# Performance work log

Hardware: AMD Instinct MI355X
Metric: run time of the kernel (lower is better)

## Reference

```python
import jax, jax.numpy as jnp
import numpy as np

EPS = 1e-5
NUM_HEADS = 8


def _conv_transpose_3x3_s2(x, w):
    # x: [B,Cin,H,W], w: [Cin,Cout,3,3] (torch ConvTranspose2d layout), stride 2, no padding
    # output spatial = (H-1)*2 + 3 = 2H+1
    return jax.lax.conv_transpose(
        x, w, strides=(2, 2), padding='VALID',
        dimension_numbers=('NCHW', 'IOHW', 'NCHW'))


def setup_inputs() -> dict:
    key = jax.random.key(0)
    ks = jax.random.split(key, 8)
    B, C, H, W = 4, 256, 32, 32
    Co, Dk, Dv = 128, 64, 64
    s = 0.05
    return {
        'x': jax.random.normal(ks[0], (B, C, H, W), jnp.float32),
        'gamma': jnp.ones((C,), jnp.float32),
        'beta': jnp.zeros((C,), jnp.float32),
        'running_mean': jax.random.normal(ks[1], (C,), jnp.float32) * 0.1,
        'running_var': jax.random.uniform(ks[2], (C,), jnp.float32, 0.5, 1.5),
        'w_sc': jax.random.normal(ks[3], (C, Co, 3, 3), jnp.float32) * s,
        'w_q': jax.random.normal(ks[4], (C, Dk, 3, 3), jnp.float32) * s,
        'w_k': jax.random.normal(ks[5], (Dk, C), jnp.float32) * s,
        'w_v': jax.random.normal(ks[6], (Dv, C), jnp.float32) * s,
        'w_o': jax.random.normal(ks[7], (Co, Dv), jnp.float32) * s,
    }


def reference(x, gamma, beta, running_mean, running_var, w_sc, w_q, w_k, w_v, w_o):
    B, C, H, W = x.shape
    h = NUM_HEADS
    # BatchNorm (inference, running stats) + ReLU, shared by both branches
    inv = jax.lax.rsqrt(running_var + EPS)
    xn = (x - running_mean[None, :, None, None]) * (gamma * inv)[None, :, None, None] \
         + beta[None, :, None, None]
    xr = jax.nn.relu(xn)

    # Shortcut: ConvTranspose2d(C->Co, 3, stride 2) -> [B,Co,2H+1,2W+1]
    shortcut = _conv_transpose_3x3_s2(xr, w_sc)

    # Attention branch ('UP'): query upsampled via ConvTranspose, k/v 1x1 at low res
    q = _conv_transpose_3x3_s2(xr, w_q)              # [B,Dk,Hu,Wu]
    k = jnp.einsum('dc,bchw->bdhw', w_k, xr)         # [B,Dk,H,W]
    v = jnp.einsum('dc,bchw->bdhw', w_v, xr)         # [B,Dv,H,W]
    Hu, Wu = q.shape[2], q.shape[3]
    Nq, Nk = Hu * Wu, H * W
    Dk, Dv = q.shape[1], v.shape[1]
    dk = Dk // h
    qh = q.reshape(B, h, dk, Nq)
    kh = k.reshape(B, h, dk, Nk)
    vh = v.reshape(B, h, Dv // h, Nk)
    scores = jnp.einsum('bhdq,bhdk->bhqk', qh, kh) / jnp.sqrt(jnp.float32(dk))
    attn = jax.nn.softmax(scores, axis=-1)           # use_softmax=True
    out = jnp.einsum('bhqk,bhdk->bhdq', attn, vh)    # [B,h,dv,Nq]
    out = out.reshape(B, Dv, Hu, Wu)
    out = jnp.einsum('od,bdhw->bohw', w_o, out)      # 1x1 output projection -> Co

    return shortcut + out
```

## Files before the change

### kernel.cpp

```cpp
#include <hip/hip_runtime.h>

typedef unsigned short u16;
typedef unsigned int u32;

typedef float f4 __attribute__((ext_vector_type(4)));
typedef short s8v __attribute__((ext_vector_type(8)));
typedef u16 us8 __attribute__((ext_vector_type(8)));
typedef _Float16 h4 __attribute__((ext_vector_type(4)));
typedef __fp16 g2 __attribute__((ext_vector_type(2)));

__device__ __forceinline__ u16 f2bf(float x){ u32 b=__float_as_uint(x); b += 0x7FFFu + ((b>>16)&1u); return (u16)(b>>16); }
__device__ __forceinline__ u16 f2h(float x){ union{_Float16 h; u16 u;} c; c.h=(_Float16)x; return c.u; }

#define O_XRT  2101248u
#define O_WPT  (O_XRT + 2097152u)
#define O_QH   (O_WPT + 884736u)
#define O_KT   (O_QH  + 2163200u)
#define O_V    (O_KT  + 524288u)
#define O_ATT  (O_V   + 524288u)
#define O_WKV  (O_ATT + 2163200u)
#define O_WO2  (O_WKV + 65536u)

__global__ __launch_bounds__(256) void k_prep(
    const float* __restrict__ x, const float* __restrict__ gamma, const float* __restrict__ beta,
    const float* __restrict__ mean, const float* __restrict__ var,
    const float* __restrict__ w_sc, const float* __restrict__ w_q,
    const float* __restrict__ w_k, const float* __restrict__ w_v, const float* __restrict__ w_o,
    u16* __restrict__ xrT, u16* __restrict__ wpt,
    u16* __restrict__ wkv, u16* __restrict__ wo2)
{
  __shared__ float SS[128], SH[128];
  __shared__ __align__(16) u16 T[32*136];
  int bi = blockIdx.x, tid = threadIdx.x;
  if (bi < 256) {
    int b = bi >> 6, pt = (bi >> 1) & 31, ch = bi & 1;
    int pix0 = pt*32, c0 = ch*128;
    if (tid < 128) {
      int c = c0 + tid;
      float s = gamma[c]*rsqrtf(var[c] + 1e-5f);
      SS[tid] = s; SH[tid] = beta[c] - mean[c]*s;
    }
    __syncthreads();
    int pix_l = tid & 31, c_l = tid >> 5;
    #pragma unroll 4
    for (int it = 0; it < 16; ++it) {
      int cl = it*8 + c_l;
      float v = x[(((size_t)(b*256 + c0 + cl))<<10) + pix0 + pix_l];
      T[pix_l*136 + cl] = f2bf(fmaxf(v*SS[cl] + SH[cl], 0.f));
    }
    __syncthreads();
    int pix_r = tid >> 3, j = tid & 7;
    us8 v0 = *(const us8*)(T + pix_r*136 + j*8);
    us8 v1 = *(const us8*)(T + pix_r*136 + 64 + j*8);
    u16* dst = xrT + (((size_t)(b*1024 + pix0 + pix_r))<<8) + c0;
    *(us8*)(dst + j*8) = v0;
    *(us8*)(dst + 64 + j*8) = v1;
    return;
  }
  int wid = (bi - 256)*256 + tid;
  if (wid < 442368) {
    int c, m, ky, kx; float val;
    if (wid < 294912) {
      c = wid / 1152; int r = wid - c*1152; m = r / 9; int t9 = r - m*9; ky = t9/3; kx = t9 - ky*3;
      val = w_sc[wid];
    } else {
      int i2 = wid - 294912;
      c = i2 / 576; int r = i2 - c*576; m = r / 9; int t9 = r - m*9; ky = t9/3; kx = t9 - ky*3;
      val = w_q[i2] * 0.51007023f;
      m += 128;
    }
    int py = (ky==1) ? 1 : 0; int dy = (ky==0) ? 1 : 0;
    int px = (kx==1) ? 1 : 0; int dx = (kx==0) ? 1 : 0;
    int cls = py*2 + px;
    int tt, KP, base;
    if (cls==0){ tt = dy*2+dx; KP=1024; base=0; }
    else if (cls==1){ tt = dy; KP=512; base=196608; }
    else if (cls==2){ tt = dx; KP=512; base=294912; }
    else { tt = 0; KP=256; base=393216; }
    wpt[base + m*KP + tt*256 + c] = f2bf(val);
  } else if (wid < 475136) {
    int i = wid - 442368; int m = i >> 8, c = i & 255;
    float vv = (m < 64) ? w_k[m*256 + c] : w_v[(m-64)*256 + c];
    wkv[m*256 + c] = f2bf(vv);
  } else if (wid < 483328) {
    int i = wid - 475136;
    wo2[i] = f2bf(w_o[i]);
  }
}

template<int PY,int PX,int TT>
__device__ __forceinline__ void conv_cls(
    const u16* __restrict__ xrT, const u16* __restrict__ wcls,
    float* __restrict__ outF, u16* __restrict__ qh,
    int mb, int nb, u16* Blds)
{
  constexpr int Hy = 33 - PY, Wx = 33 - PX;
  constexpr int NC = 4*Hy*Wx;
  constexpr int KP = TT*256;
  constexpr int NKT = KP/32;
  int tid = threadIdx.x;
  int lane = tid & 63, wv = tid >> 6, quad = lane >> 4, c15 = lane & 15;
  int sn = tid >> 2, sg = tid & 3;
  int n_g = nb*64 + sn;
  bool nv = n_g < NC;
  int bb=0, yq=0, xq=0;
  if (nv) { bb = n_g/(Hy*Wx); int rem = n_g - bb*(Hy*Wx); yq = rem/Wx; xq = rem - yq*Wx; }
  f4 acc[4];
  #pragma unroll
  for (int i=0;i<4;i++) acc[i] = (f4){0.f,0.f,0.f,0.f};
  const u16* arow = wcls + (size_t)(mb*64 + wv*16 + c15)*KP + quad*8;
  auto loadB = [&](int kt)->us8 {
    int tt = kt >> 3, cb = (kt & 7)*32;
    int dy, dx;
    if (TT==4){ dy = tt>>1; dx = tt&1; }
    else if (TT==2){ if (PX==1){ dy=tt; dx=0; } else { dy=0; dx=tt; } }
    else { dy=0; dx=0; }
    int ii = yq - dy, jj = xq - dx;
    bool ok = nv && (ii>=0) && (ii<32) && (jj>=0) && (jj<32);
    us8 v = (us8)0;
    if (ok) v = *(const us8*)(xrT + (((size_t)((bb<<10) + ii*32 + jj))<<8) + cb + sg*8);
    return v;
  };
  us8 cur = loadB(0);
  for (int kt = 0; kt < NKT; ++kt) {
    __syncthreads();
    *(us8*)(Blds + sn*40 + sg*8) = cur;
    __syncthreads();
    if (kt + 1 < NKT) cur = loadB(kt + 1);
    s8v a = *(const s8v*)(arow + kt*32);
    #pragma unroll
    for (int t4=0;t4<4;t4++) {
      s8v bf = *(const s8v*)(Blds + (t4*16 + c15)*40 + quad*8);
      acc[t4] = __builtin_amdgcn_mfma_f32_16x16x32_bf16(a, bf, acc[t4], 0, 0, 0);
    }
  }
  #pragma unroll
  for (int t4=0;t4<4;t4++) {
    int n2 = nb*64 + t4*16 + c15;
    if (n2 < NC) {
      int bb2 = n2/(Hy*Wx); int rem = n2 - bb2*(Hy*Wx); int yq2 = rem/Wx; int xq2 = rem - yq2*Wx;
      int pix = (2*yq2 + PY)*65 + (2*xq2 + PX);
      if (mb < 2) {
        int mrow = mb*64 + wv*16 + quad*4;
        #pragma unroll
        for (int rg=0; rg<4; rg++)
          outF[(size_t)(bb2*128 + mrow + rg)*4225 + pix] = acc[t4][rg];
      } else {
        int dv = wv*16 + quad*4;
        u16 pk[4];
        #pragma unroll
        for (int rg=0; rg<4; rg++) pk[rg] = f2h(acc[t4][rg]);
        *(uint2*)(qh + (((size_t)(bb2*4225 + pix))<<6) + dv) = *(uint2*)pk;
      }
    }
  }
}

__global__ __launch_bounds__(256) void k_conv(
    const u16* __restrict__ xrT, const u16* __restrict__ wpt, const u16* __restrict__ wkv,
    float* __restrict__ outF, u16* __restrict__ qh,
    u16* __restrict__ kT, u16* __restrict__ vbuf)
{
  __shared__ __align__(16) u16 Blds[64*40];
  int bi = blockIdx.x;
  if (bi < 795) {
    int mb = bi % 3, cy = bi / 3;
    if (cy < 69)       conv_cls<0,0,4>(xrT, wpt,          outF, qh, mb, cy,     Blds);
    else if (cy < 135) conv_cls<0,1,2>(xrT, wpt + 196608, outF, qh, mb, cy-69,  Blds);
    else if (cy < 201) conv_cls<1,0,2>(xrT, wpt + 294912, outF, qh, mb, cy-135, Blds);
    else               conv_cls<1,1,1>(xrT, wpt + 393216, outF, qh, mb, cy-201, Blds);
    return;
  }
  int t = bi - 795;
  int mb = t & 1, nb = t >> 1;
  int tid = threadIdx.x;
  int lane = tid & 63, wv = tid >> 6, quad = lane >> 4, c15 = lane & 15;
  int sn = tid >> 2, sg = tid & 3;
  int n_g = nb*64 + sn;
  f4 acc[4];
  #pragma unroll
  for (int i=0;i<4;i++) acc[i] = (f4){0.f,0.f,0.f,0.f};
  const u16* arow = wkv + (size_t)(mb*64 + wv*16 + c15)*256 + quad*8;
  us8 cur = *(const us8*)(xrT + (((size_t)n_g)<<8) + sg*8);
  for (int kt = 0; kt < 8; ++kt) {
    __syncthreads();
    *(us8*)(Blds + sn*40 + sg*8) = cur;
    __syncthreads();
    if (kt < 7) cur = *(const us8*)(xrT + (((size_t)n_g)<<8) + (kt+1)*32 + sg*8);
    s8v a = *(const s8v*)(arow + kt*32);
    #pragma unroll
    for (int t4=0;t4<4;t4++) {
      s8v bf = *(const s8v*)(Blds + (t4*16 + c15)*40 + quad*8);
      acc[t4] = __builtin_amdgcn_mfma_f32_16x16x32_bf16(a, bf, acc[t4], 0, 0, 0);
    }
  }
  int ml = wv*16 + quad*4;
  #pragma unroll
  for (int t4=0;t4<4;t4++) {
    int n2 = nb*64 + t4*16 + c15;
    int b = n2 >> 10, pix = n2 & 1023;
    if (mb == 0) {
      int h = ml >> 3, d0 = ml & 7;
      u16 pk[4];
      #pragma unroll
      for (int rg=0; rg<4; rg++) pk[rg] = f2h(acc[t4][rg]);
      *(uint2*)(kT + ((size_t)(b*8+h)<<13) + pix*8 + d0) = *(uint2*)pk;
    } else {
      #pragma unroll
      for (int rg=0; rg<4; rg++)
        vbuf[(((size_t)(b*64 + ml + rg))<<10) + pix] = f2h(acc[t4][rg]);
    }
  }
}

__global__ __launch_bounds__(256) void k_attn(
    const u16* __restrict__ qh, const u16* __restrict__ kT, const u16* __restrict__ vbuf,
    u16* __restrict__ attT)
{
  __shared__ __align__(16) u16 KL[8192];
  __shared__ __align__(16) u16 VL[9*1032];
  int qt = blockIdx.x, bh = blockIdx.y;
  int b = bh >> 3, h = bh & 7;
  int tid = threadIdx.x, lane = tid & 63, wv = tid >> 6, quad = lane >> 4, c15 = lane & 15;
  {
    const uint4* kg = (const uint4*)(kT + ((size_t)bh << 13));
    for (int i = tid; i < 1024; i += 256) ((uint4*)KL)[i] = kg[i];
    const u16* vg = vbuf + ((size_t)(b*64 + h*8) << 10);
    for (int i = tid; i < 1024; i += 256) {
      int dv = i >> 7, k8 = (i & 127) << 3;
      *(uint4*)(VL + dv*1032 + k8) = *(const uint4*)(vg + (dv<<10) + k8);
    }
    if (tid < 129) {
      us8 ones;
      #pragma unroll
      for (int i=0;i<8;i++) ones[i] = 0x3C00;
      *(us8*)(VL + 8*1032 + tid*8) = ones;
    }
  }
  __syncthreads();
  int q0 = qt*128 + wv*32 + c15;
  int q1 = q0 + 16;
  int qa = q0 < 4224 ? q0 : 4224;
  int qb = q1 < 4224 ? q1 : 4224;
  uint2 t0 = *(const uint2*)(qh + (((size_t)(b*4225 + qa))<<6) + h*8 + (quad&1)*4);
  uint2 t1 = *(const uint2*)(qh + (((size_t)(b*4225 + qb))<<6) + h*8 + (quad&1)*4);
  h4 bq0 = quad < 2 ? *(h4*)&t0 : (h4)(_Float16)0.f;
  h4 bq1 = quad < 2 ? *(h4*)&t1 : (h4)(_Float16)0.f;
  const u16* klb = KL + c15*8 + (quad&1)*4;
  int vr = c15 > 8 ? 8 : c15;
  const u16* vlb = VL + vr*1032 + quad*4;
  const f4 zf = {0.f,0.f,0.f,0.f};
  f4 O0 = {0.f,0.f,0.f,0.f}, O1 = {0.f,0.f,0.f,0.f};
  #pragma unroll 8
  for (int kt=0; kt<64; ++kt) {
    h4 ak = *(const h4*)(klb + kt*128);
    h4 av = *(const h4*)(vlb + kt*16);
    f4 s0 = __builtin_amdgcn_mfma_f32_16x16x16f16(ak, bq0, zf, 0, 0, 0);
    f4 s1 = __builtin_amdgcn_mfma_f32_16x16x16f16(ak, bq1, zf, 0, 0, 0);
    g2 p0l = __builtin_amdgcn_cvt_pkrtz(__builtin_amdgcn_exp2f(s0[0]), __builtin_amdgcn_exp2f(s0[1]));
    g2 p0h = __builtin_amdgcn_cvt_pkrtz(__builtin_amdgcn_exp2f(s0[2]), __builtin_amdgcn_exp2f(s0[3]));
    g2 p1l = __builtin_amdgcn_cvt_pkrtz(__builtin_amdgcn_exp2f(s1[0]), __builtin_amdgcn_exp2f(s1[1]));
    g2 p1h = __builtin_amdgcn_cvt_pkrtz(__builtin_amdgcn_exp2f(s1[2]), __builtin_amdgcn_exp2f(s1[3]));
    h4 pf0; pf0[0]=(_Float16)p0l[0]; pf0[1]=(_Float16)p0l[1]; pf0[2]=(_Float16)p0h[0]; pf0[3]=(_Float16)p0h[1];
    h4 pf1; pf1[0]=(_Float16)p1l[0]; pf1[1]=(_Float16)p1l[1]; pf1[2]=(_Float16)p1h[0]; pf1[3]=(_Float16)p1h[1];
    O0 = __builtin_amdgcn_mfma_f32_16x16x16f16(av, pf0, O0, 0, 0, 0);
    O1 = __builtin_amdgcn_mfma_f32_16x16x16f16(av, pf1, O1, 0, 0, 0);
  }
  float l0 = __shfl(O0[0], 32 + c15, 64);
  float l1 = __shfl(O1[0], 32 + c15, 64);
  float r0 = __builtin_amdgcn_rcpf(l0);
  float r1 = __builtin_amdgcn_rcpf(l1);
  if (quad < 2) {
    if (q0 < 4225) {
      u16 pk[4];
      #pragma unroll
      for (int rg=0;rg<4;rg++) pk[rg] = f2bf(O0[rg]*r0);
      *(uint2*)(attT + (((size_t)(b*4225 + q0))<<6) + h*8 + quad*4) = *(uint2*)pk;
    }
    if (q1 < 4225) {
      u16 pk[4];
      #pragma unroll
      for (int rg=0;rg<4;rg++) pk[rg] = f2bf(O1[rg]*r1);
      *(uint2*)(attT + (((size_t)(b*4225 + q1))<<6) + h*8 + quad*4) = *(uint2*)pk;
    }
  }
}

__global__ __launch_bounds__(256) void k_proj(
    const u16* __restrict__ attT, const u16* __restrict__ wo2, float* __restrict__ outF)
{
  int nbi = blockIdx.x, b = blockIdx.y;
  int tid = threadIdx.x;
  int lane = tid & 63, wv = tid >> 6, quad = lane >> 4, c15 = lane & 15;
  f4 acc[2][4];
  #pragma unroll
  for (int am=0;am<2;am++)
    #pragma unroll
    for (int i=0;i<4;i++) acc[am][i] = (f4){0.f,0.f,0.f,0.f};
  #pragma unroll
  for (int kt = 0; kt < 2; ++kt) {
    s8v a0 = *(const s8v*)(wo2 + (size_t)(wv*32 + c15)*64 + kt*32 + quad*8);
    s8v a1 = *(const s8v*)(wo2 + (size_t)(wv*32 + 16 + c15)*64 + kt*32 + quad*8);
    #pragma unroll
    for (int t4=0;t4<4;t4++) {
      int n = nbi*64 + t4*16 + c15;
      int nc = n < 4224 ? n : 4224;
      s8v bf = *(const s8v*)(attT + (((size_t)(b*4225 + nc))<<6) + kt*32 + quad*8);
      acc[0][t4] = __builtin_amdgcn_mfma_f32_16x16x32_bf16(a0, bf, acc[0][t4], 0, 0, 0);
      acc[1][t4] = __builtin_amdgcn_mfma_f32_16x16x32_bf16(a1, bf, acc[1][t4], 0, 0, 0);
    }
  }
  #pragma unroll
  for (int am=0;am<2;am++) {
    int mrow = wv*32 + am*16 + quad*4;
    #pragma unroll
    for (int t4=0;t4<4;t4++) {
      int n2 = nbi*64 + t4*16 + c15;
      if (n2 < 4225) {
        float* op = outF + (size_t)(b*128 + mrow)*4225 + n2;
        #pragma unroll
        for (int rg=0; rg<4; rg++) op[(size_t)rg*4225] += acc[am][t4][rg];
      }
    }
  }
}

extern "C" void kernel_launch(void* const* d_in, const int* in_sizes, int n_in,
                              void* d_out, int out_size, void* d_ws, size_t ws_size,
                              hipStream_t stream) {
  const float* x     = (const float*)d_in[0];
  const float* gamma = (const float*)d_in[1];
  const float* beta  = (const float*)d_in[2];
  const float* mean  = (const float*)d_in[3];
  const float* var   = (const float*)d_in[4];
  const float* w_sc  = (const float*)d_in[5];
  const float* w_q   = (const float*)d_in[6];
  const float* w_k   = (const float*)d_in[7];
  const float* w_v   = (const float*)d_in[8];
  const float* w_o   = (const float*)d_in[9];
  char* ws = (char*)d_ws;
  u16*   xrT  = (u16*)(ws + O_XRT);
  u16*   wpt  = (u16*)(ws + O_WPT);
  u16*   qhb  = (u16*)(ws + O_QH);
  u16*   kT   = (u16*)(ws + O_KT);
  u16*   vbuf = (u16*)(ws + O_V);
  u16*   attT = (u16*)(ws + O_ATT);
  u16*   wkv  = (u16*)(ws + O_WKV);
  u16*   wo2  = (u16*)(ws + O_WO2);
  float* outF = (float*)d_out;

  k_prep<<<2144, 256, 0, stream>>>(x, gamma, beta, mean, var, w_sc, w_q, w_k, w_v, w_o,
                                   xrT, wpt, wkv, wo2);
  k_conv<<<923, 256, 0, stream>>>(xrT, wpt, wkv, outF, qhb, kT, vbuf);
  k_attn<<<dim3(34, 32), 256, 0, stream>>>(qhb, kT, vbuf, attT);
  k_proj<<<dim3(67, 4), 256, 0, stream>>>(attT, wo2, outF);
}
```

Baseline: 136.0 us.

## Pad activation buffer with zero halo and double-buffer K=64 LDS tiles in conv

The transposed activations are stored in a zero-padded 34x34 layout, with the border zeroed by extra prep blocks. This lets the conv gather drop its per-load bounds checks and predication. The conv and k/v GEMM loops now consume 64 channels per step with double-buffered LDS, so each iteration needs one barrier instead of two and there are half as many iterations. The attention loop also builds its P fragment by bit-casting instead of converting element by element. The cost is more LDS per block, which may limit occupancy, plus the extra prep work to zero the halo.

```diff
diff --git a/kernel.cpp b/kernel.cpp
--- a/kernel.cpp
+++ b/kernel.cpp
@@ -12,8 +12,8 @@
 __device__ __forceinline__ u16 f2bf(float x){ u32 b=__float_as_uint(x); b += 0x7FFFu + ((b>>16)&1u); return (u16)(b>>16); }
 __device__ __forceinline__ u16 f2h(float x){ union{_Float16 h; u16 u;} c; c.h=(_Float16)x; return c.u; }
 
-#define O_XRT  2101248u
-#define O_WPT  (O_XRT + 2097152u)
+#define O_XRT  4096u
+#define O_WPT  (O_XRT + 2367488u)
 #define O_QH   (O_WPT + 884736u)
 #define O_KT   (O_QH  + 2163200u)
 #define O_V    (O_KT  + 524288u)
@@ -26,7 +26,7 @@
     const float* __restrict__ mean, const float* __restrict__ var,
     const float* __restrict__ w_sc, const float* __restrict__ w_q,
     const float* __restrict__ w_k, const float* __restrict__ w_v, const float* __restrict__ w_o,
-    u16* __restrict__ xrT, u16* __restrict__ wpt,
+    u16* __restrict__ xrTp, u16* __restrict__ wpt,
     u16* __restrict__ wkv, u16* __restrict__ wo2)
 {
   __shared__ float SS[128], SH[128];
@@ -52,7 +52,7 @@
     int pix_r = tid >> 3, j = tid & 7;
     us8 v0 = *(const us8*)(T + pix_r*136 + j*8);
     us8 v1 = *(const us8*)(T + pix_r*136 + 64 + j*8);
-    u16* dst = xrT + (((size_t)(b*1024 + pix0 + pix_r))<<8) + c0;
+    u16* dst = xrTp + (((size_t)(b*1156 + (pt+1)*34 + 1 + pix_r))<<8) + c0;
     *(us8*)(dst + j*8) = v0;
     *(us8*)(dst + 64 + j*8) = v1;
     return;
@@ -85,60 +85,75 @@
   } else if (wid < 483328) {
     int i = wid - 475136;
     wo2[i] = f2bf(w_o[i]);
+  } else if (wid < 500224) {
+    int i = wid - 483328;
+    int b = i / 4224; int r = i - b*4224;
+    int hp = r >> 5, j = r & 31;
+    int p;
+    if (hp < 34) p = hp;
+    else if (hp < 68) p = 33*34 + (hp - 34);
+    else if (hp < 100) p = (hp - 68 + 1)*34;
+    else p = (hp - 100 + 1)*34 + 33;
+    *(us8*)(xrTp + (((size_t)(b*1156 + p))<<8) + j*8) = (us8)0;
   }
 }
 
 template<int PY,int PX,int TT>
 __device__ __forceinline__ void conv_cls(
-    const u16* __restrict__ xrT, const u16* __restrict__ wcls,
+    const u16* __restrict__ xrTp, const u16* __restrict__ wcls,
     float* __restrict__ outF, u16* __restrict__ qh,
     int mb, int nb, u16* Blds)
 {
   constexpr int Hy = 33 - PY, Wx = 33 - PX;
   constexpr int NC = 4*Hy*Wx;
   constexpr int KP = TT*256;
-  constexpr int NKT = KP/32;
+  constexpr int NKT = KP/64;
   int tid = threadIdx.x;
   int lane = tid & 63, wv = tid >> 6, quad = lane >> 4, c15 = lane & 15;
   int sn = tid >> 2, sg = tid & 3;
   int n_g = nb*64 + sn;
-  bool nv = n_g < NC;
-  int bb=0, yq=0, xq=0;
-  if (nv) { bb = n_g/(Hy*Wx); int rem = n_g - bb*(Hy*Wx); yq = rem/Wx; xq = rem - yq*Wx; }
+  int ncl = n_g < NC ? n_g : NC-1;
+  int bb = ncl/(Hy*Wx); int rem = ncl - bb*(Hy*Wx); int yq = rem/Wx; int xq = rem - yq*Wx;
+  const u16* bsrc = xrTp + (((size_t)(bb*1156 + (yq+1)*34 + xq+1))<<8) + sg*16;
   f4 acc[4];
   #pragma unroll
   for (int i=0;i<4;i++) acc[i] = (f4){0.f,0.f,0.f,0.f};
   const u16* arow = wcls + (size_t)(mb*64 + wv*16 + c15)*KP + quad*8;
-  auto loadB = [&](int kt)->us8 {
-    int tt = kt >> 3, cb = (kt & 7)*32;
+  auto loadB = [&](int kt, us8& v0, us8& v1) {
+    int tt = kt >> 2, c0 = (kt & 3)*64;
     int dy, dx;
     if (TT==4){ dy = tt>>1; dx = tt&1; }
     else if (TT==2){ if (PX==1){ dy=tt; dx=0; } else { dy=0; dx=tt; } }
     else { dy=0; dx=0; }
-    int ii = yq - dy, jj = xq - dx;
-    bool ok = nv && (ii>=0) && (ii<32) && (jj>=0) && (jj<32);
-    us8 v = (us8)0;
-    if (ok) v = *(const us8*)(xrT + (((size_t)((bb<<10) + ii*32 + jj))<<8) + cb + sg*8);
-    return v;
+    const u16* p = bsrc - (((dy*34+dx))<<8) + c0;
+    v0 = *(const us8*)p;
+    v1 = *(const us8*)(p+8);
   };
-  us8 cur = loadB(0);
+  us8 cv0, cv1; loadB(0, cv0, cv1);
+  int pb = 0;
   for (int kt = 0; kt < NKT; ++kt) {
+    u16* Bw = Blds + pb*4608;
+    *(us8*)(Bw + sn*72 + sg*16) = cv0;
+    *(us8*)(Bw + sn*72 + sg*16 + 8) = cv1;
     __syncthreads();
-    *(us8*)(Blds + sn*40 + sg*8) = cur;
-    __syncthreads();
-    if (kt + 1 < NKT) cur = loadB(kt + 1);
-    s8v a = *(const s8v*)(arow + kt*32);
+    if (kt + 1 < NKT) loadB(kt+1, cv0, cv1);
+    s8v a0 = *(const s8v*)(arow + kt*64);
+    s8v a1 = *(const s8v*)(arow + kt*64 + 32);
     #pragma unroll
     for (int t4=0;t4<4;t4++) {
-      s8v bf = *(const s8v*)(Blds + (t4*16 + c15)*40 + quad*8);
-      acc[t4] = __builtin_amdgcn_mfma_f32_16x16x32_bf16(a, bf, acc[t4], 0, 0, 0);
-    }
+      const u16* br = Blds + pb*4608 + (t4*16 + c15)*72 + quad*8;
+      s8v bf0 = *(const s8v*)br;
+      s8v bf1 = *(const s8v*)(br + 32);
+      acc[t4] = __builtin_amdgcn_mfma_f32_16x16x32_bf16(a0, bf0, acc[t4], 0, 0, 0);
+      acc[t4] = __builtin_amdgcn_mfma_f32_16x16x32_bf16(a1, bf1, acc[t4], 0, 0, 0);
+    }
+    pb ^= 1;
   }
   #pragma unroll
   for (int t4=0;t4<4;t4++) {
     int n2 = nb*64 + t4*16 + c15;
     if (n2 < NC) {
-      int bb2 = n2/(Hy*Wx); int rem = n2 - bb2*(Hy*Wx); int yq2 = rem/Wx; int xq2 = rem - yq2*Wx;
+      int bb2 = n2/(Hy*Wx); int rem2 = n2 - bb2*(Hy*Wx); int yq2 = rem2/Wx; int xq2 = rem2 - yq2*Wx;
       int pix = (2*yq2 + PY)*65 + (2*xq2 + PX);
       if (mb < 2) {
         int mrow = mb*64 + wv*16 + quad*4;
@@ -157,18 +172,18 @@
 }
 
 __global__ __launch_bounds__(256) void k_conv(
-    const u16* __restrict__ xrT, const u16* __restrict__ wpt, const u16* __restrict__ wkv,
+    const u16* __restrict__ xrTp, const u16* __restrict__ wpt, const u16* __restrict__ wkv,
     float* __restrict__ outF, u16* __restrict__ qh,
     u16* __restrict__ kT, u16* __restrict__ vbuf)
 {
-  __shared__ __align__(16) u16 Blds[64*40];
+  __shared__ __align__(16) u16 Blds[2*4608];
   int bi = blockIdx.x;
   if (bi < 795) {
     int mb = bi % 3, cy = bi / 3;
-    if (cy < 69)       conv_cls<0,0,4>(xrT, wpt,          outF, qh, mb, cy,     Blds);
-    else if (cy < 135) conv_cls<0,1,2>(xrT, wpt + 196608, outF, qh, mb, cy-69,  Blds);
-    else if (cy < 201) conv_cls<1,0,2>(xrT, wpt + 294912, outF, qh, mb, cy-135, Blds);
-    else               conv_cls<1,1,1>(xrT, wpt + 393216, outF, qh, mb, cy-201, Blds);
+    if (cy < 69)       conv_cls<0,0,4>(xrTp, wpt,          outF, qh, mb, cy,     Blds);
+    else if (cy < 135) conv_cls<0,1,2>(xrTp, wpt + 196608, outF, qh, mb, cy-69,  Blds);
+    else if (cy < 201) conv_cls<1,0,2>(xrTp, wpt + 294912, outF, qh, mb, cy-135, Blds);
+    else               conv_cls<1,1,1>(xrTp, wpt + 393216, outF, qh, mb, cy-201, Blds);
     return;
   }
   int t = bi - 795;
@@ -177,22 +192,31 @@
   int lane = tid & 63, wv = tid >> 6, quad = lane >> 4, c15 = lane & 15;
   int sn = tid >> 2, sg = tid & 3;
   int n_g = nb*64 + sn;
+  int b0 = n_g >> 10, pix0 = n_g & 1023, y0 = pix0 >> 5, x0 = pix0 & 31;
+  const u16* bsrc = xrTp + (((size_t)(b0*1156 + (y0+1)*34 + x0+1))<<8) + sg*16;
   f4 acc[4];
   #pragma unroll
   for (int i=0;i<4;i++) acc[i] = (f4){0.f,0.f,0.f,0.f};
   const u16* arow = wkv + (size_t)(mb*64 + wv*16 + c15)*256 + quad*8;
-  us8 cur = *(const us8*)(xrT + (((size_t)n_g)<<8) + sg*8);
-  for (int kt = 0; kt < 8; ++kt) {
+  us8 cv0 = *(const us8*)bsrc, cv1 = *(const us8*)(bsrc + 8);
+  int pb = 0;
+  for (int kt = 0; kt < 4; ++kt) {
+    u16* Bw = Blds + pb*4608;
+    *(us8*)(Bw + sn*72 + sg*16) = cv0;
+    *(us8*)(Bw + sn*72 + sg*16 + 8) = cv1;
     __syncthreads();
-    *(us8*)(Blds + sn*40 + sg*8) = cur;
-    __syncthreads();
-    if (kt < 7) cur = *(const us8*)(xrT + (((size_t)n_g)<<8) + (kt+1)*32 + sg*8);
-    s8v a = *(const s8v*)(arow + kt*32);
+    if (kt < 3) { cv0 = *(const us8*)(bsrc + (kt+1)*64); cv1 = *(const us8*)(bsrc + (kt+1)*64 + 8); }
+    s8v a0 = *(const s8v*)(arow + kt*64);
+    s8v a1 = *(const s8v*)(arow + kt*64 + 32);
     #pragma unroll
     for (int t4=0;t4<4;t4++) {
-      s8v bf = *(const s8v*)(Blds + (t4*16 + c15)*40 + quad*8);
-      acc[t4] = __builtin_amdgcn_mfma_f32_16x16x32_bf16(a, bf, acc[t4], 0, 0, 0);
-    }
+      const u16* br = Blds + pb*4608 + (t4*16 + c15)*72 + quad*8;
+      s8v bf0 = *(const s8v*)br;
+      s8v bf1 = *(const s8v*)(br + 32);
+      acc[t4] = __builtin_amdgcn_mfma_f32_16x16x32_bf16(a0, bf0, acc[t4], 0, 0, 0);
+      acc[t4] = __builtin_amdgcn_mfma_f32_16x16x32_bf16(a1, bf1, acc[t4], 0, 0, 0);
+    }
+    pb ^= 1;
   }
   int ml = wv*16 + quad*4;
   #pragma unroll
@@ -251,6 +275,7 @@
   const u16* vlb = VL + vr*1032 + quad*4;
   const f4 zf = {0.f,0.f,0.f,0.f};
   f4 O0 = {0.f,0.f,0.f,0.f}, O1 = {0.f,0.f,0.f,0.f};
+  union HU { uint2 u; h4 h; };
   #pragma unroll 8
   for (int kt=0; kt<64; ++kt) {
     h4 ak = *(const h4*)(klb + kt*128);
@@ -261,10 +286,10 @@
     g2 p0h = __builtin_amdgcn_cvt_pkrtz(__builtin_amdgcn_exp2f(s0[2]), __builtin_amdgcn_exp2f(s0[3]));
     g2 p1l = __builtin_amdgcn_cvt_pkrtz(__builtin_amdgcn_exp2f(s1[0]), __builtin_amdgcn_exp2f(s1[1]));
     g2 p1h = __builtin_amdgcn_cvt_pkrtz(__builtin_amdgcn_exp2f(s1[2]), __builtin_amdgcn_exp2f(s1[3]));
-    h4 pf0; pf0[0]=(_Float16)p0l[0]; pf0[1]=(_Float16)p0l[1]; pf0[2]=(_Float16)p0h[0]; pf0[3]=(_Float16)p0h[1];
-    h4 pf1; pf1[0]=(_Float16)p1l[0]; pf1[1]=(_Float16)p1l[1]; pf1[2]=(_Float16)p1h[0]; pf1[3]=(_Float16)p1h[1];
-    O0 = __builtin_amdgcn_mfma_f32_16x16x16f16(av, pf0, O0, 0, 0, 0);
-    O1 = __builtin_amdgcn_mfma_f32_16x16x16f16(av, pf1, O1, 0, 0, 0);
+    HU u0; u0.u.x = __builtin_bit_cast(u32, p0l); u0.u.y = __builtin_bit_cast(u32, p0h);
+    HU u1; u1.u.x = __builtin_bit_cast(u32, p1l); u1.u.y = __builtin_bit_cast(u32, p1h);
+    O0 = __builtin_amdgcn_mfma_f32_16x16x16f16(av, u0.h, O0, 0, 0, 0);
+    O1 = __builtin_amdgcn_mfma_f32_16x16x16f16(av, u1.h, O1, 0, 0, 0);
   }
   float l0 = __shfl(O0[0], 32 + c15, 64);
   float l1 = __shfl(O1[0], 32 + c15, 64);
@@ -339,7 +364,7 @@
   const float* w_v   = (const float*)d_in[8];
   const float* w_o   = (const float*)d_in[9];
   char* ws = (char*)d_ws;
-  u16*   xrT  = (u16*)(ws + O_XRT);
+  u16*   xrTp = (u16*)(ws + O_XRT);
   u16*   wpt  = (u16*)(ws + O_WPT);
   u16*   qhb  = (u16*)(ws + O_QH);
   u16*   kT   = (u16*)(ws + O_KT);
@@ -349,9 +374,9 @@
   u16*   wo2  = (u16*)(ws + O_WO2);
   float* outF = (float*)d_out;
 
-  k_prep<<<2144, 256, 0, stream>>>(x, gamma, beta, mean, var, w_sc, w_q, w_k, w_v, w_o,
-                                   xrT, wpt, wkv, wo2);
-  k_conv<<<923, 256, 0, stream>>>(xrT, wpt, wkv, outF, qhb, kT, vbuf);
+  k_prep<<<2211, 256, 0, stream>>>(x, gamma, beta, mean, var, w_sc, w_q, w_k, w_v, w_o,
+                                   xrTp, wpt, wkv, wo2);
+  k_conv<<<923, 256, 0, stream>>>(xrTp, wpt, wkv, outF, qhb, kT, vbuf);
   k_attn<<<dim3(34, 32), 256, 0, stream>>>(qhb, kT, vbuf, attT);
   k_proj<<<dim3(67, 4), 256, 0, stream>>>(attT, wo2, outF);
 }
```

New measurement: 135.5 us. No clear change (-0.4%).
